# Kernel tuning notes

Measured on AMD Instinct MI355X. Metric: run time of the kernel, lower is better.

The kernel has to match this reference:

```python
import jax, jax.numpy as jnp
import numpy as np
from functools import partial

# Module hyperparameters (from init_kwargs)
T, C_IN, H, W_DIM = 128, 16, 64, 64
C_OUT, KH, KW = 64, 3, 3
PAD = ((1, 1), (1, 1))  # (top,bottom),(left,right) -> symmetric here
STRIDES = (1, 1)
F_V_THRESH = 8.0
F_V_THRESH_LOW = -1.0
F_V_RESET = 0.0
# fVSubtract is None -> reset-to-value branch


def setup_inputs() -> dict:
    key = jax.random.key(0)
    kx, kw, kb = jax.random.split(key, 3)
    x = jax.random.uniform(kx, (T, C_IN, H, W_DIM), dtype=jnp.float32)
    fan_in = C_IN * KH * KW
    bound = 1.0 / np.sqrt(fan_in)
    W = jax.random.uniform(kw, (C_OUT, C_IN, KH, KW), dtype=jnp.float32,
                           minval=-bound, maxval=bound)
    b = jax.random.uniform(kb, (C_OUT,), dtype=jnp.float32,
                           minval=-bound, maxval=bound)
    return {"x": x, "W": W, "b": b}


def _spiking_conv(x, W, b):
    # conv over all timesteps at once (time is the conv batch dim): [T, C_out, H, W]
    conv_out = jax.lax.conv_general_dilated(
        x, W, window_strides=STRIDES, padding=PAD,
        dimension_numbers=("NCHW", "OIHW", "NCHW"))
    conv_out = conv_out + b[None, :, None, None]

    def step(state, conv_t):
        state = state + conv_t
        spikes = (state >= F_V_THRESH).astype(conv_t.dtype)
        # reset-to-value branch (fVSubtract is None)
        state = spikes * F_V_RESET + state * (1.0 - spikes)
        # nn.Threshold(v, v): x if x > v else v
        state = jnp.where(state > F_V_THRESH_LOW, state, F_V_THRESH_LOW)
        return state, spikes

    init_state = jnp.zeros(conv_out.shape[1:], dtype=conv_out.dtype)
    _, num_spikes = jax.lax.scan(step, init_state, conv_out)
    return num_spikes  # [T, C_out, H, W] float (0/1)


def reference(x, W, b):
    return _spiking_conv(x, W, b)
```

## Files before the change

kernel.cpp:

```cpp
#include <hip/hip_runtime.h>

#define T_STEPS 128
#define CIN     16
#define HH      64
#define WW      64
#define COUT    64
#define HWSZ    (HH * WW)
#define CHW     (COUT * HWSZ)
#define XCHW    (CIN * HWSZ)

#define TILE    32
#define HALO    34
#define LSTR    36
#define PLANE   (HALO * LSTR)
#define NST     (CIN * HALO * HALO)
#define WBLK    40

__global__ void transpose_w(const float* __restrict__ W, float* __restrict__ Wtr) {
    int e = blockIdx.x * 256 + threadIdx.x;
    if (e >= COUT * CIN * 9) return;
    int co = e / (CIN * 9);
    int r  = e - co * (CIN * 9);
    int ci = r / 9;
    int k  = r - ci * 9;
    Wtr[((co >> 2) * CIN + ci) * WBLK + (co & 3) * 9 + k] = W[e];
}

__global__ __launch_bounds__(512, 4)
void spiking_conv_pass1(const float* __restrict__ x, const float* __restrict__ Wtr,
                        const float* __restrict__ b, float* __restrict__ out) {
    __shared__ float xs[CIN * PLANE];

    const int tid = threadIdx.x;
    const int t   = blockIdx.y;
    const int h0  = (blockIdx.x >> 1) * TILE;
    const int w0  = (blockIdx.x & 1) * TILE;
    const int coh = blockIdx.z;

    const float* xt = x + t * XCHW;
    {
        float vbuf[19]; int ibuf[19];
#pragma unroll
        for (int k = 0; k < 18; ++k) {
            unsigned e = tid + k * 512;
            unsigned ci = e / (HALO * HALO);
            unsigned rem = e - ci * (HALO * HALO);
            unsigned r  = rem / HALO;
            unsigned c  = rem - r * HALO;
            int gh = h0 - 1 + (int)r;
            int gw = w0 - 1 + (int)c;
            bool inb = (unsigned)gh < HH && (unsigned)gw < WW;
            vbuf[k] = inb ? xt[ci * HWSZ + gh * WW + gw] : 0.f;
            ibuf[k] = ci * PLANE + r * LSTR + c;
        }
#pragma unroll
        for (int k = 0; k < 18; ++k) xs[ibuf[k]] = vbuf[k];
#pragma unroll
        for (int k = 0; k < 19; ++k) {
            unsigned e = tid + (18 + k) * 512;
            unsigned ci = e / (HALO * HALO);
            unsigned rem = e - ci * (HALO * HALO);
            unsigned r  = rem / HALO;
            unsigned c  = rem - r * HALO;
            int gh = h0 - 1 + (int)r;
            int gw = w0 - 1 + (int)c;
            bool inb = e < NST && (unsigned)gh < HH && (unsigned)gw < WW;
            vbuf[k] = inb ? xt[ci * HWSZ + gh * WW + gw] : 0.f;
            ibuf[k] = (e < NST) ? (int)(ci * PLANE + r * LSTR + c) : -1;
        }
#pragma unroll
        for (int k = 0; k < 19; ++k)
            if (ibuf[k] >= 0) xs[ibuf[k]] = vbuf[k];
    }
    __syncthreads();

    const int cog = __builtin_amdgcn_readfirstlane(tid >> 8);
    const int sp  = tid & 255;
    const int pr0 = sp >> 3;
    const int pc0 = (sp & 7) * 4;
    float* outt = out + t * CHW;

    float acc[16][4];
#pragma unroll
    for (int j = 0; j < 16; ++j)
#pragma unroll
        for (int p = 0; p < 4; ++p) acc[j][p] = 0.f;

#pragma unroll 1
    for (int ci = 0; ci < CIN; ++ci) {
        float xv[3][6];
#pragma unroll
        for (int dr = 0; dr < 3; ++dr) {
            const float* row = &xs[ci * PLANE + (pr0 + dr) * LSTR + pc0];
            float4 a  = *(const float4*)row;
            float2 c2 = *(const float2*)(row + 4);
            xv[dr][0] = a.x;  xv[dr][1] = a.y;
            xv[dr][2] = a.z;  xv[dr][3] = a.w;
            xv[dr][4] = c2.x; xv[dr][5] = c2.y;
        }
#pragma unroll
        for (int g = 0; g < 4; ++g) {
            const int g4 = coh * 8 + cog * 4 + g;
            const float* wb = Wtr + (g4 * CIN + ci) * WBLK;
            float w[36];
#pragma unroll
            for (int i = 0; i < 36; ++i) w[i] = wb[i];
#pragma unroll
            for (int jj = 0; jj < 4; ++jj)
#pragma unroll
                for (int ky = 0; ky < 3; ++ky)
#pragma unroll
                    for (int kx = 0; kx < 3; ++kx) {
                        const float wv = w[jj * 9 + ky * 3 + kx];
#pragma unroll
                        for (int p = 0; p < 4; ++p)
                            acc[g * 4 + jj][p] += wv * xv[ky][kx + p];
                    }
        }
    }

#pragma unroll
    for (int g = 0; g < 4; ++g)
#pragma unroll
        for (int jj = 0; jj < 4; ++jj) {
            const int co = coh * 32 + cog * 16 + g * 4 + jj;
            const float bias = b[co];
            float4 o;
            o.x = acc[g * 4 + jj][0] + bias;
            o.y = acc[g * 4 + jj][1] + bias;
            o.z = acc[g * 4 + jj][2] + bias;
            o.w = acc[g * 4 + jj][3] + bias;
            *(float4*)&outt[co * HWSZ + (h0 + pr0) * WW + (w0 + pc0)] = o;
        }
}

__global__ __launch_bounds__(256)
void spiking_scan_pass2(float* __restrict__ io) {
    const int idx = blockIdx.x * 256 + threadIdx.x;
    float4* p = (float4*)io + idx;
    float sx = 0.f, sy = 0.f, sz = 0.f, sw = 0.f;
    float4 v[8], nv[8];
#pragma unroll
    for (int i = 0; i < 8; ++i) v[i] = p[(size_t)i * (CHW / 4)];
#pragma unroll 1
    for (int tb = 0; tb < 15; ++tb) {
#pragma unroll
        for (int i = 0; i < 8; ++i) nv[i] = p[(size_t)((tb + 1) * 8 + i) * (CHW / 4)];
#pragma unroll
        for (int i = 0; i < 8; ++i) {
            float4 o;
            sx += v[i].x; bool a0 = (sx >= 8.0f); o.x = a0 ? 1.f : 0.f; sx = a0 ? 0.f : sx; sx = fmaxf(sx, -1.f);
            sy += v[i].y; bool a1 = (sy >= 8.0f); o.y = a1 ? 1.f : 0.f; sy = a1 ? 0.f : sy; sy = fmaxf(sy, -1.f);
            sz += v[i].z; bool a2 = (sz >= 8.0f); o.z = a2 ? 1.f : 0.f; sz = a2 ? 0.f : sz; sz = fmaxf(sz, -1.f);
            sw += v[i].w; bool a3 = (sw >= 8.0f); o.w = a3 ? 1.f : 0.f; sw = a3 ? 0.f : sw; sw = fmaxf(sw, -1.f);
            p[(size_t)(tb * 8 + i) * (CHW / 4)] = o;
        }
#pragma unroll
        for (int i = 0; i < 8; ++i) v[i] = nv[i];
    }
#pragma unroll
    for (int i = 0; i < 8; ++i) {
        float4 o;
        sx += v[i].x; bool a0 = (sx >= 8.0f); o.x = a0 ? 1.f : 0.f; sx = a0 ? 0.f : sx; sx = fmaxf(sx, -1.f);
        sy += v[i].y; bool a1 = (sy >= 8.0f); o.y = a1 ? 1.f : 0.f; sy = a1 ? 0.f : sy; sy = fmaxf(sy, -1.f);
        sz += v[i].z; bool a2 = (sz >= 8.0f); o.z = a2 ? 1.f : 0.f; sz = a2 ? 0.f : sz; sz = fmaxf(sz, -1.f);
        sw += v[i].w; bool a3 = (sw >= 8.0f); o.w = a3 ? 1.f : 0.f; sw = a3 ? 0.f : sw; sw = fmaxf(sw, -1.f);
        p[(size_t)(120 + i) * (CHW / 4)] = o;
    }
}

extern "C" void kernel_launch(void* const* d_in, const int* in_sizes, int n_in,
                              void* d_out, int out_size, void* d_ws, size_t ws_size,
                              hipStream_t stream) {
    const float* x = (const float*)d_in[0];
    const float* W = (const float*)d_in[1];
    const float* b = (const float*)d_in[2];
    float* out = (float*)d_out;
    float* Wtr = (float*)d_ws;

    transpose_w<<<36, 256, 0, stream>>>(W, Wtr);

    dim3 g1(4, 128, 2);
    spiking_conv_pass1<<<g1, 512, 0, stream>>>(x, Wtr, b, out);

    spiking_scan_pass2<<<(CHW / 4) / 256, 256, 0, stream>>>(out);
}
```

Measured before the change: 266.9 us.

## Split conv by channel half, use separate workspace buffer and nontemporal scan stores

The conv launch over both output-channel halves is split into two sequential launches, each covering one half. Conv results now go to a workspace buffer when it is large enough, instead of being written into the output. The scan reads from that buffer and writes spikes to the output with nontemporal stores, separating read and write streams and avoiding cache pollution. The trade-offs are an extra launch, a 128 MB workspace footprint, and a smaller grid per conv launch.

```diff
diff --git a/kernel.cpp b/kernel.cpp
--- a/kernel.cpp
+++ b/kernel.cpp
@@ -16,6 +16,8 @@
 #define NST     (CIN * HALO * HALO)
 #define WBLK    40
 
+typedef float vfloat4 __attribute__((ext_vector_type(4)));
+
 __global__ void transpose_w(const float* __restrict__ W, float* __restrict__ Wtr) {
     int e = blockIdx.x * 256 + threadIdx.x;
     if (e >= COUT * CIN * 9) return;
@@ -28,14 +30,14 @@
 
 __global__ __launch_bounds__(512, 4)
 void spiking_conv_pass1(const float* __restrict__ x, const float* __restrict__ Wtr,
-                        const float* __restrict__ b, float* __restrict__ out) {
+                        const float* __restrict__ b, float* __restrict__ out,
+                        const int coh) {
     __shared__ float xs[CIN * PLANE];
 
     const int tid = threadIdx.x;
     const int t   = blockIdx.y;
     const int h0  = (blockIdx.x >> 1) * TILE;
     const int w0  = (blockIdx.x & 1) * TILE;
-    const int coh = blockIdx.z;
 
     const float* xt = x + t * XCHW;
     {
@@ -135,37 +137,38 @@
 }
 
 __global__ __launch_bounds__(256)
-void spiking_scan_pass2(float* __restrict__ io) {
+void spiking_scan_pass2(const float* __restrict__ src, float* __restrict__ dst) {
     const int idx = blockIdx.x * 256 + threadIdx.x;
-    float4* p = (float4*)io + idx;
+    const float4* ps = (const float4*)src + idx;
+    vfloat4* pd = (vfloat4*)dst + idx;
     float sx = 0.f, sy = 0.f, sz = 0.f, sw = 0.f;
     float4 v[8], nv[8];
 #pragma unroll
-    for (int i = 0; i < 8; ++i) v[i] = p[(size_t)i * (CHW / 4)];
+    for (int i = 0; i < 8; ++i) v[i] = ps[(size_t)i * (CHW / 4)];
 #pragma unroll 1
     for (int tb = 0; tb < 15; ++tb) {
 #pragma unroll
-        for (int i = 0; i < 8; ++i) nv[i] = p[(size_t)((tb + 1) * 8 + i) * (CHW / 4)];
+        for (int i = 0; i < 8; ++i) nv[i] = ps[(size_t)((tb + 1) * 8 + i) * (CHW / 4)];
 #pragma unroll
         for (int i = 0; i < 8; ++i) {
-            float4 o;
+            vfloat4 o;
             sx += v[i].x; bool a0 = (sx >= 8.0f); o.x = a0 ? 1.f : 0.f; sx = a0 ? 0.f : sx; sx = fmaxf(sx, -1.f);
             sy += v[i].y; bool a1 = (sy >= 8.0f); o.y = a1 ? 1.f : 0.f; sy = a1 ? 0.f : sy; sy = fmaxf(sy, -1.f);
             sz += v[i].z; bool a2 = (sz >= 8.0f); o.z = a2 ? 1.f : 0.f; sz = a2 ? 0.f : sz; sz = fmaxf(sz, -1.f);
             sw += v[i].w; bool a3 = (sw >= 8.0f); o.w = a3 ? 1.f : 0.f; sw = a3 ? 0.f : sw; sw = fmaxf(sw, -1.f);
-            p[(size_t)(tb * 8 + i) * (CHW / 4)] = o;
+            __builtin_nontemporal_store(o, &pd[(size_t)(tb * 8 + i) * (CHW / 4)]);
         }
 #pragma unroll
         for (int i = 0; i < 8; ++i) v[i] = nv[i];
     }
 #pragma unroll
     for (int i = 0; i < 8; ++i) {
-        float4 o;
+        vfloat4 o;
         sx += v[i].x; bool a0 = (sx >= 8.0f); o.x = a0 ? 1.f : 0.f; sx = a0 ? 0.f : sx; sx = fmaxf(sx, -1.f);
         sy += v[i].y; bool a1 = (sy >= 8.0f); o.y = a1 ? 1.f : 0.f; sy = a1 ? 0.f : sy; sy = fmaxf(sy, -1.f);
         sz += v[i].z; bool a2 = (sz >= 8.0f); o.z = a2 ? 1.f : 0.f; sz = a2 ? 0.f : sz; sz = fmaxf(sz, -1.f);
         sw += v[i].w; bool a3 = (sw >= 8.0f); o.w = a3 ? 1.f : 0.f; sw = a3 ? 0.f : sw; sw = fmaxf(sw, -1.f);
-        p[(size_t)(120 + i) * (CHW / 4)] = o;
+        __builtin_nontemporal_store(o, &pd[(size_t)(120 + i) * (CHW / 4)]);
     }
 }
 
@@ -178,10 +181,16 @@
     float* out = (float*)d_out;
     float* Wtr = (float*)d_ws;
 
+    const size_t CONV_BYTES = (size_t)T_STEPS * CHW * sizeof(float);
+    const size_t CONV_OFF   = 1u << 20;
+    const bool   big_ws     = ws_size >= CONV_OFF + CONV_BYTES;
+    float* conv = big_ws ? (float*)((char*)d_ws + CONV_OFF) : out;
+
     transpose_w<<<36, 256, 0, stream>>>(W, Wtr);
 
-    dim3 g1(4, 128, 2);
-    spiking_conv_pass1<<<g1, 512, 0, stream>>>(x, Wtr, b, out);
+    dim3 g1(4, 128, 1);
+    spiking_conv_pass1<<<g1, 512, 0, stream>>>(x, Wtr, b, conv, 0);
+    spiking_conv_pass1<<<g1, 512, 0, stream>>>(x, Wtr, b, conv, 1);
 
-    spiking_scan_pass2<<<(CHW / 4) / 256, 256, 0, stream>>>(out);
+    spiking_scan_pass2<<<(CHW / 4) / 256, 256, 0, stream>>>(conv, out);
 }
```

After: 275.7 us. 3.3% more time.
